# Optimization experiments

Measured on AMD Instinct MI355X. Metric: run time of the kernel, lower is better.

The kernel has to match this reference:

```python
import jax, jax.numpy as jnp
import numpy as np

# batch, net nodes/graph, vnr nodes/graph, hidden, static feats, vnr feats, vnf types, value out
B, NN, NV, H, FS, FV, T, O = 64, 1000, 10, 128, 8, 6, 8, 64
EN, EV = B * NN * 8, B * NV * 4  # total edges (avg degree 8 / 4)


def _gat(h, src, dst, W, al, ar, b):
    """dgl GATConv, num_heads=1, activation=None, allow_zero_in_degree=True."""
    n = h.shape[0]
    z = h @ W                                                    # [N,H]
    e = jax.nn.leaky_relu((z @ al)[src] + (z @ ar)[dst], 0.2)    # [E]
    emax = jax.ops.segment_max(e, dst, num_segments=n)
    ee = jnp.exp(e - emax[dst])
    alpha = ee / jax.ops.segment_sum(ee, dst, num_segments=n)[dst]
    return jax.ops.segment_sum(z[src] * alpha[:, None], dst, num_segments=n) + b


def _gru_cell(x, h, W_ih, W_hh, b_ih, b_hh):
    gi = x @ W_ih.T + b_ih
    gh = h @ W_hh.T + b_hh
    ir, iz, in_ = jnp.split(gi, 3, axis=-1)
    hr, hz, hn = jnp.split(gh, 3, axis=-1)
    r = jax.nn.sigmoid(ir + hr)
    z = jax.nn.sigmoid(iz + hz)
    n = jnp.tanh(in_ + r * hn)
    return (1.0 - z) * n + z * h


def _forward(static_feat, vnr_feat, nmask,
             Ws1, als1, ars1, bs1, Ws2, als2, ars2, bs2, Ws3, als3, ars3, bs3,
             Wv1, alv1, arv1, bv1, Wv2, alv2, arv2, bv2, Wv3, alv3, arv3, bv3,
             W_attn, v_attn, W_ih, W_hh, b_ih, b_hh, h0, W_out, b_out,
             src_s, dst_s, src_v, dst_v, vnr_VNF, net_VNF):
    # ---- graph encoders: 3 stacked GAT layers each ----
    hs = _gat(static_feat, src_s, dst_s, Ws1, als1, ars1, bs1)
    hs = _gat(hs, src_s, dst_s, Ws2, als2, ars2, bs2)
    hs = _gat(hs, src_s, dst_s, Ws3, als3, ars3, bs3)            # [B*NN,H]
    hv = _gat(vnr_feat, src_v, dst_v, Wv1, alv1, arv1, bv1)
    hv = _gat(hv, src_v, dst_v, Wv2, alv2, arv2, bv2)
    hv = _gat(hv, src_v, dst_v, Wv3, alv3, arv3, bv3)            # [B*NV,H]
    static_hidden = hs.reshape(B, NN, H).transpose(0, 2, 1)      # [B,H,NN]
    vnr_hidden = hv.reshape(B, NV, H).transpose(0, 2, 1)         # [B,H,NV]

    # ---- pointer decoder ----
    netV = net_VNF.reshape(B, NN, T)
    # mask[b,i,n] = netV[b, n, vnr_VNF[b,i]]
    masks = jnp.take_along_axis(netV[:, None, :, :], vnr_VNF[:, :, None, None], axis=3)[..., 0]  # [B,NV,NN]

    def step(h, x):
        h_new = _gru_cell(x, h, W_ih, W_hh, b_ih, b_hh)          # [B,H]
        cat = jnp.concatenate(
            [static_hidden, jnp.broadcast_to(h_new[:, :, None], (B, H, NN))], axis=1)  # [B,2H,NN]
        attn = jnp.einsum('h,bhn->bn', v_attn,
                          jnp.tanh(jnp.einsum('hk,bkn->bhn', W_attn, cat)))
        return h_new, attn

    h0b = jnp.broadcast_to(h0, (B, H))
    xs = vnr_hidden.transpose(2, 0, 1)                            # [NV,B,H]
    _, attns = jax.lax.scan(step, h0b, xs)                        # [NV,B,NN]
    pi = (attns.transpose(1, 0, 2) + jnp.log(masks.astype(jnp.float32))).reshape(B, -1)

    # ---- value head ----
    nm = nmask.reshape(B, NV)
    y1 = (vnr_hidden.transpose(0, 2, 1) * nm[:, :, None]).sum(1) / nm.sum(1, keepdims=True)
    y2 = static_hidden.mean(2)
    val = jnp.concatenate([y1, y2], axis=1) @ W_out.T + b_out     # [B,O]
    return pi, val


def setup_inputs() -> dict:
    key = jax.random.key(0)
    ks = iter(jax.random.split(key, 60))

    def nrm(shape, fan):
        return jax.random.normal(next(ks), shape, jnp.float32) / np.sqrt(fan).astype(np.float32)

    inp = {
        'static_feat': jax.random.normal(next(ks), (B * NN, FS), jnp.float32),
        'vnr_feat': jax.random.normal(next(ks), (B * NV, FV), jnp.float32),
        'nmask': jnp.ones((B * NV,), jnp.float32),
    }
    for pfx, fin in (('s1', FS), ('s2', H), ('s3', H), ('v1', FV), ('v2', H), ('v3', H)):
        inp['W' + pfx] = nrm((fin, H), fin)
        inp['al' + pfx] = nrm((H,), H)
        inp['ar' + pfx] = nrm((H,), H)
        inp['b' + pfx] = jnp.zeros((H,), jnp.float32)
    inp['W_attn'] = nrm((H, 2 * H), 2 * H)
    inp['v_attn'] = nrm((H,), H)
    inp['W_ih'] = nrm((3 * H, H), H)
    inp['W_hh'] = nrm((3 * H, H), H)
    inp['b_ih'] = jnp.zeros((3 * H,), jnp.float32)
    inp['b_hh'] = jnp.zeros((3 * H,), jnp.float32)
    inp['h0'] = jnp.zeros((H,), jnp.float32)
    inp['W_out'] = nrm((O, 2 * H), 2 * H)
    inp['b_out'] = jnp.zeros((O,), jnp.float32)
    inp['src_s'] = jax.random.randint(next(ks), (EN,), 0, B * NN)
    inp['dst_s'] = jax.random.randint(next(ks), (EN,), 0, B * NN)
    inp['src_v'] = jax.random.randint(next(ks), (EV,), 0, B * NV)
    inp['dst_v'] = jax.random.randint(next(ks), (EV,), 0, B * NV)
    inp['vnr_VNF'] = jax.random.randint(next(ks), (B, NV), 0, T)
    inp['net_VNF'] = jnp.ones((B * NN, T), jnp.int32)
    return inp


def reference(static_feat, vnr_feat, nmask,
              Ws1, als1, ars1, bs1, Ws2, als2, ars2, bs2, Ws3, als3, ars3, bs3,
              Wv1, alv1, arv1, bv1, Wv2, alv2, arv2, bv2, Wv3, alv3, arv3, bv3,
              W_attn, v_attn, W_ih, W_hh, b_ih, b_hh, h0, W_out, b_out,
              src_s, dst_s, src_v, dst_v, vnr_VNF, net_VNF):
    return _forward(static_feat, vnr_feat, nmask,
                    Ws1, als1, ars1, bs1, Ws2, als2, ars2, bs2, Ws3, als3, ars3, bs3,
                    Wv1, alv1, arv1, bv1, Wv2, alv2, arv2, bv2, Wv3, alv3, arv3, bv3,
                    W_attn, v_attn, W_ih, W_hh, b_ih, b_hh, h0, W_out, b_out,
                    src_s, dst_s, src_v, dst_v, vnr_VNF, net_VNF)
```

## Files before the change

### kernel.cpp

```cpp
#include <hip/hip_runtime.h>
#include <hip/hip_bf16.h>
#include <math.h>

#define B_   64
#define NN_  1000
#define NV_  10
#define H_   128
#define FS_  8
#define FV_  6
#define T_   8
#define O_   64
#define EN_  512000
#define EV_  2560
#define NS_  (B_*NN_)
#define NVT_ (B_*NV_)

typedef __attribute__((ext_vector_type(8))) short short8v;
typedef __attribute__((ext_vector_type(4))) float floatx4;

__device__ __forceinline__ float fast_rcp(float x) { return __builtin_amdgcn_rcpf(x); }
__device__ __forceinline__ float fast_tanh(float x) {
  return 1.f - 2.f*fast_rcp(1.f + __expf(2.f*x));
}
__device__ __forceinline__ float fast_sigmoid(float x) {
  return fast_rcp(1.f + __expf(-x));
}
__device__ __forceinline__ unsigned short bf16_rne(float x) {
  unsigned u = __float_as_uint(x);
  return (unsigned short)((u + 0x7FFFu + ((u >> 16) & 1u)) >> 16);
}
__device__ __forceinline__ float bf16_tof(unsigned short b) {
  return __uint_as_float(((unsigned)b) << 16);
}
__device__ __forceinline__ float dot4(float4 a, float4 b) {
  return a.x*b.x + a.y*b.y + a.z*b.z + a.w*b.w;
}
__device__ __forceinline__ float lrelu02(float e) {
  return (e > 0.f) ? e : 0.2f*e;
}

__global__ __launch_bounds__(256) void k_count(const int* dst, int E, int* counts) {
  int i = blockIdx.x*256 + threadIdx.x;
  if (i < E) atomicAdd(&counts[dst[i]], 1);
}

__global__ __launch_bounds__(1024) void k_scan(const int* cnt, int n, int* rowptr) {
  __shared__ int sums[1024];
  int t = threadIdx.x;
  int v = (t < n) ? cnt[t] : 0;
  sums[t] = v;
  __syncthreads();
  for (int offd = 1; offd < 1024; offd <<= 1) {
    int u = (t >= offd) ? sums[t-offd] : 0;
    __syncthreads();
    sums[t] += u;
    __syncthreads();
  }
  if (t < n) rowptr[t] = sums[t] - v;
  if (t == n-1) rowptr[n] = sums[t];
}

__global__ __launch_bounds__(256) void k_scan_local(const int* cnt, int n, int* out, int* bsum) {
  __shared__ int s[256];
  int t = threadIdx.x; int i = blockIdx.x*256 + t;
  int v = (i < n) ? cnt[i] : 0;
  s[t] = v; __syncthreads();
  #pragma unroll
  for (int o = 1; o < 256; o <<= 1) {
    int u = (t >= o) ? s[t-o] : 0; __syncthreads();
    s[t] += u; __syncthreads();
  }
  if (i < n) out[i] = s[t] - v;
  if (t == 255) bsum[blockIdx.x] = s[255];
}

__global__ __launch_bounds__(256) void k_scan_bsum(int* bsum, int nb) {
  __shared__ int s[256];
  int t = threadIdx.x;
  int v = (t < nb) ? bsum[t] : 0;
  s[t] = v; __syncthreads();
  #pragma unroll
  for (int o = 1; o < 256; o <<= 1) {
    int u = (t >= o) ? s[t-o] : 0; __syncthreads();
    s[t] += u; __syncthreads();
  }
  if (t < nb) bsum[t] = s[t] - v;
}

__global__ __launch_bounds__(256) void k_scan_add(int* out, const int* bsum, int n, int E) {
  int i = blockIdx.x*256 + threadIdx.x;
  if (i < n) out[i] += bsum[blockIdx.x];
  if (i == 0) out[n] = E;
}

__global__ __launch_bounds__(256) void k_scatter(const int* src, const int* dst, int E,
                                                 const int* rowptr, int* cursor,
                                                 unsigned short* srcp) {
  int i = blockIdx.x*256 + threadIdx.x;
  if (i >= E) return;
  int d = dst[i];
  int pos = rowptr[d] + atomicAdd(&cursor[d], 1);
  srcp[pos] = (unsigned short)src[i];
}

__global__ __launch_bounds__(256) void k_aggregate_v(int nNodes, const int* __restrict__ rowptr,
    const unsigned short* __restrict__ srcp, const float* __restrict__ el,
    const float* __restrict__ er, const float* __restrict__ z,
    const float* __restrict__ bias, float* __restrict__ out) {
  int w = (blockIdx.x*256 + threadIdx.x) >> 6;
  int lane = threadIdx.x & 63;
  if (w >= nNodes) return;
  int beg = rowptr[w], end = rowptr[w+1];
  float erw = er[w];
  float a0 = 0.f, a1 = 0.f, wsum = 0.f;
  for (int i = beg; i < end; ++i) {
    int sI = srcp[i];
    float wt = __expf(lrelu02(el[sI] + erw));
    float2 zz = *(const float2*)(z + (size_t)sI*H_ + lane*2);
    a0 += wt*zz.x; a1 += wt*zz.y; wsum += wt;
  }
  float inv = (end > beg) ? fast_rcp(wsum) : 0.f;
  float2 o;
  o.x = a0*inv + bias[lane*2];
  o.y = a1*inv + bias[lane*2 + 1];
  *(float2*)(out + (size_t)w*H_ + lane*2) = o;
}

__global__ __launch_bounds__(256) void k_aggregate_split(int nNodes, const int* __restrict__ rowptr,
    const unsigned short* __restrict__ srcp, const float* __restrict__ el, const float* __restrict__ er,
    const unsigned short* __restrict__ z, const float* __restrict__ bias,
    unsigned short* __restrict__ outHi, unsigned short* __restrict__ outLo) {
  int w = (blockIdx.x*256 + threadIdx.x) >> 6;
  int lane = threadIdx.x & 63;
  if (w >= nNodes) return;
  int beg = rowptr[w], end = rowptr[w+1];
  float erw = er[w];
  float a0 = 0.f, a1 = 0.f, wsum = 0.f;
  int i = beg;
  for (; i + 8 <= end; i += 8) {
    int sI[8]; float lv[8]; ushort2 q[8];
    #pragma unroll
    for (int u = 0; u < 8; ++u) sI[u] = srcp[i+u];
    #pragma unroll
    for (int u = 0; u < 8; ++u) lv[u] = el[sI[u]];
    #pragma unroll
    for (int u = 0; u < 8; ++u) q[u] = *(const ushort2*)(z + (size_t)sI[u]*H_ + lane*2);
    #pragma unroll
    for (int u = 0; u < 8; ++u) {
      float wt = __expf(lrelu02(lv[u] + erw));
      a0 += wt*bf16_tof(q[u].x);
      a1 += wt*bf16_tof(q[u].y);
      wsum += wt;
    }
  }
  for (; i < end; ++i) {
    int sI = srcp[i];
    float wt = __expf(lrelu02(el[sI] + erw));
    ushort2 q = *(const ushort2*)(z + (size_t)sI*H_ + lane*2);
    a0 += wt*bf16_tof(q.x); a1 += wt*bf16_tof(q.y); wsum += wt;
  }
  float inv = (end > beg) ? fast_rcp(wsum) : 0.f;
  float o0 = a0*inv + bias[lane*2];
  float o1 = a1*inv + bias[lane*2 + 1];
  unsigned short h0 = bf16_rne(o0), h1 = bf16_rne(o1);
  unsigned short l0 = bf16_rne(o0 - bf16_tof(h0)), l1 = bf16_rne(o1 - bf16_tof(h1));
  ushort2 hv; hv.x = h0; hv.y = h1;
  ushort2 lv; lv.x = l0; lv.y = l1;
  *(ushort2*)(outHi + (size_t)w*H_ + lane*2) = hv;
  *(ushort2*)(outLo + (size_t)w*H_ + lane*2) = lv;
}

__global__ __launch_bounds__(256) void k_prep(const float* W_ih, const float* Ws2,
                                              const float* Ws3, const float* W_attn,
                                              float* WTih,
                                              unsigned short* WS2hi, unsigned short* WS2lo,
                                              unsigned short* WS3hi, unsigned short* WS3lo,
                                              unsigned short* WAhi, unsigned short* WAlo) {
  int idx = blockIdx.x*256 + threadIdx.x;
  int task = blockIdx.y;
  if (task == 0) {
    if (idx < 128*384) {
      int k = idx / 384, j = idx - k*384;
      WTih[idx] = W_ih[(size_t)j*128 + k];
    }
  } else {
    if (idx >= 128*128) return;
    int j = idx >> 7, k = idx & 127;
    float v; unsigned short *hi, *lo;
    if (task == 1)      { v = Ws2[(size_t)k*128 + j];    hi = WS2hi; lo = WS2lo; }
    else if (task == 2) { v = Ws3[(size_t)k*128 + j];    hi = WS3hi; lo = WS3lo; }
    else                { v = W_attn[(size_t)j*256 + k]; hi = WAhi;  lo = WAlo;  }
    unsigned short h = bf16_rne(v);
    hi[idx] = h; lo[idx] = bf16_rne(v - bf16_tof(h));
  }
}

__global__ __launch_bounds__(256) void k_mfma_gemm(
    const unsigned short* __restrict__ Ahi, const unsigned short* __restrict__ Alo,
    const unsigned short* __restrict__ WThi, const unsigned short* __restrict__ WTlo,
    float* __restrict__ C, unsigned short* __restrict__ Cb,
    const float* __restrict__ al, const float* __restrict__ ar,
    float* __restrict__ el, float* __restrict__ er) {
  __shared__ unsigned short lAhi[64*136];
  __shared__ unsigned short lAlo[64*136];
  __shared__ float redl[4][64];
  __shared__ float redr[4][64];
  int t = threadIdx.x;
  int row0 = blockIdx.x * 64;
  int wid = t >> 6, lane = t & 63;
  int g = lane >> 4, c = lane & 15;

  #pragma unroll
  for (int i = 0; i < 4; ++i) {
    int m = t + 256*i;
    int r = m >> 4;
    int kc = (m & 15) * 8;
    *(short8v*)(lAhi + r*136 + kc) = *(const short8v*)(Ahi + (size_t)(row0 + r)*H_ + kc);
    *(short8v*)(lAlo + r*136 + kc) = *(const short8v*)(Alo + (size_t)(row0 + r)*H_ + kc);
  }

  short8v bhi[2][4], blo[2][4];
  #pragma unroll
  for (int ct = 0; ct < 2; ++ct) {
    int col = wid*32 + ct*16 + c;
    #pragma unroll
    for (int kb = 0; kb < 4; ++kb) {
      size_t o = (size_t)col*H_ + kb*32 + g*8;
      bhi[ct][kb] = *(const short8v*)(WThi + o);
      blo[ct][kb] = *(const short8v*)(WTlo + o);
    }
  }

  floatx4 acc[4][2];
  #pragma unroll
  for (int rt = 0; rt < 4; ++rt)
    #pragma unroll
    for (int ct = 0; ct < 2; ++ct)
      acc[rt][ct] = (floatx4){0.f, 0.f, 0.f, 0.f};

  __syncthreads();

  #pragma unroll
  for (int kb = 0; kb < 4; ++kb) {
    short8v ahi[4], alo[4];
    #pragma unroll
    for (int rt = 0; rt < 4; ++rt) {
      int r = rt*16 + c;
      ahi[rt] = *(const short8v*)(lAhi + r*136 + kb*32 + g*8);
      alo[rt] = *(const short8v*)(lAlo + r*136 + kb*32 + g*8);
    }
    #pragma unroll
    for (int rt = 0; rt < 4; ++rt)
      #pragma unroll
      for (int ct = 0; ct < 2; ++ct) {
        acc[rt][ct] = __builtin_amdgcn_mfma_f32_16x16x32_bf16(ahi[rt], bhi[ct][kb], acc[rt][ct], 0, 0, 0);
        acc[rt][ct] = __builtin_amdgcn_mfma_f32_16x16x32_bf16(alo[rt], bhi[ct][kb], acc[rt][ct], 0, 0, 0);
        acc[rt][ct] = __builtin_amdgcn_mfma_f32_16x16x32_bf16(ahi[rt], blo[ct][kb], acc[rt][ct], 0, 0, 0);
      }
  }

  #pragma unroll
  for (int rt = 0; rt < 4; ++rt)
    #pragma unroll
    for (int i = 0; i < 4; ++i) {
      int row = row0 + rt*16 + g*4 + i;
      if (Cb) {
        unsigned short* cr = Cb + (size_t)row*H_ + wid*32;
        cr[c]      = bf16_rne(acc[rt][0][i]);
        cr[16 + c] = bf16_rne(acc[rt][1][i]);
      } else {
        float* cr = C + (size_t)row*H_ + wid*32;
        cr[c]      = acc[rt][0][i];
        cr[16 + c] = acc[rt][1][i];
      }
    }

  if (el) {
    float av0 = al[wid*32 + c], av1 = al[wid*32 + 16 + c];
    float rv0 = ar[wid*32 + c], rv1 = ar[wid*32 + 16 + c];
    #pragma unroll
    for (int rt = 0; rt < 4; ++rt)
      #pragma unroll
      for (int i = 0; i < 4; ++i) {
        float pl = acc[rt][0][i]*av0 + acc[rt][1][i]*av1;
        float pr = acc[rt][0][i]*rv0 + acc[rt][1][i]*rv1;
        pl += __shfl_xor(pl, 1, 64); pl += __shfl_xor(pl, 2, 64);
        pl += __shfl_xor(pl, 4, 64); pl += __shfl_xor(pl, 8, 64);
        pr += __shfl_xor(pr, 1, 64); pr += __shfl_xor(pr, 2, 64);
        pr += __shfl_xor(pr, 4, 64); pr += __shfl_xor(pr, 8, 64);
        if (c == 0) { redl[wid][rt*16 + g*4 + i] = pl; redr[wid][rt*16 + g*4 + i] = pr; }
      }
    __syncthreads();
    if (t < 64) {
      el[row0 + t] = redl[0][t] + redl[1][t] + redl[2][t] + redl[3][t];
      er[row0 + t] = redr[0][t] + redr[1][t] + redr[2][t] + redr[3][t];
    }
  }
}

__global__ __launch_bounds__(256) void k_gemm(const float* A, int M, int K, int N,
                                              const float* W, const float* bias,
                                              float* C, unsigned short* Cb,
                                              const float* al, const float* ar,
                                              float* el, float* er) {
  __shared__ float Ws_[64*128];
  __shared__ float As_[16*128];
  __shared__ float redl[16][17];
  __shared__ float redr[16][17];
  int t = threadIdx.x;
  int j0 = blockIdx.y * 128;
  int row0 = blockIdx.x * 16;
  for (int l = t; l < 16*K; l += 256) {
    int r = l / K, k = l - r*K;
    int row = row0 + r;
    As_[r*K + k] = (row < M) ? A[(size_t)row*K + k] : 0.f;
  }
  int jg = t & 15, r = t >> 4;
  float acc[8];
  #pragma unroll
  for (int q = 0; q < 8; ++q) acc[q] = 0.f;
  for (int kc = 0; kc < K; kc += 64) {
    int kl = min(64, K - kc);
    __syncthreads();
    for (int l = t; l < (kl << 7); l += 256) {
      int k = l >> 7, j = l & 127;
      int jj = j0 + j;
      Ws_[l] = (jj < N) ? W[(size_t)(kc + k)*N + jj] : 0.f;
    }
    __syncthreads();
    for (int k = 0; k < kl; ++k) {
      float a = As_[r*K + kc + k];
      const float* wr = &Ws_[(k << 7) + jg*8];
      #pragma unroll
      for (int q = 0; q < 8; ++q) acc[q] += a * wr[q];
    }
  }
  int row = row0 + r;
  if (row < M) {
    if (Cb) {
      unsigned short* crow = Cb + (size_t)row*N + j0 + jg*8;
      #pragma unroll
      for (int q = 0; q < 8; ++q) {
        int j = j0 + jg*8 + q;
        if (j < N) crow[q] = bf16_rne(acc[q] + (bias ? bias[j] : 0.f));
      }
    } else {
      float* crow = C + (size_t)row*N + j0 + jg*8;
      #pragma unroll
      for (int q = 0; q < 8; ++q) {
        int j = j0 + jg*8 + q;
// ... 86 lines not shown
  int b = blockIdx.y;
  int t = threadIdx.x;
  for (int i = t; i < 1280; i += 256) {
    int s = i >> 7, k = i & 127;
    a2s[s][k] = 2.f*A2[((size_t)s*B_ + b)*H_ + k];
  }
  if (t < 128) vv2s[t] = 2.f*v_attn[t];
  __syncthreads();
  int nl = t >> 2, p = t & 3;
  int n = blockIdx.x*64 + nl;
  if (n >= NN_) return;
  size_t g = (size_t)b*NN_ + n;
  const float4* arow = (const float4*)(A1 + g*H_ + p*32);
  float4 a[8], w2[8];
  #pragma unroll
  for (int kk = 0; kk < 8; ++kk) {
    float4 av = arow[kk];
    a[kk] = make_float4(2.f*av.x, 2.f*av.y, 2.f*av.z, 2.f*av.w);
    w2[kk] = *(const float4*)(&vv2s[p*32 + kk*4]);
  }
  float vsum = 0.f;
  #pragma unroll
  for (int kk = 0; kk < 8; ++kk)
    vsum += (w2[kk].x + w2[kk].y) + (w2[kk].z + w2[kk].w);
  vsum *= 0.5f;
  float acc[10];
  #pragma unroll
  for (int s = 0; s < 10; ++s) {
    const float* a2r = &a2s[s][p*32];
    float sum2 = 0.f;
    #pragma unroll
    for (int kk = 0; kk < 8; ++kk) {
      float4 c = *(const float4*)(a2r + kk*4);
      sum2 = fmaf(w2[kk].x, fast_rcp(1.f + __expf(a[kk].x + c.x)), sum2);
      sum2 = fmaf(w2[kk].y, fast_rcp(1.f + __expf(a[kk].y + c.y)), sum2);
      sum2 = fmaf(w2[kk].z, fast_rcp(1.f + __expf(a[kk].z + c.z)), sum2);
      sum2 = fmaf(w2[kk].w, fast_rcp(1.f + __expf(a[kk].w + c.w)), sum2);
    }
    acc[s] = vsum - sum2;
  }
  #pragma unroll
  for (int s = 0; s < 10; ++s) {
    acc[s] += __shfl_xor(acc[s], 1, 64);
    acc[s] += __shfl_xor(acc[s], 2, 64);
  }
  if (p == 0) {
    #pragma unroll
    for (int s = 0; s < 10; ++s) {
      int vnf = vnr_VNF[b*NV_ + s];
      int m   = net_VNF[g*T_ + vnf];
      pi[(size_t)b*(NV_*NN_) + (size_t)s*NN_ + n] = acc[s] + __logf((float)m);
    }
  }
}

__global__ __launch_bounds__(128) void k_y2s(const unsigned short* hi, const unsigned short* lo,
                                             float* y2) {
  int b = blockIdx.x, slice = blockIdx.y, h = threadIdx.x;
  int n0 = slice*125, n1 = n0 + 125;
  float s = 0.f;
  for (int n = n0; n < n1; ++n) {
    size_t idx = ((size_t)b*NN_ + n)*H_ + h;
    s += bf16_tof(hi[idx]) + bf16_tof(lo[idx]);
  }
  atomicAdd(&y2[b*H_ + h], s);
}

__global__ __launch_bounds__(128) void k_value(const float* __restrict__ Hv,
                                               const float* __restrict__ nmask,
                                               const float* __restrict__ y2,
                                               const float* __restrict__ W_out,
                                               const float* __restrict__ b_out,
                                               float* __restrict__ val) {
  __shared__ float y1s[128];
  int b = blockIdx.x, t = threadIdx.x;
  float s = 0.f, d = 0.f;
  #pragma unroll
  for (int i = 0; i < NV_; ++i) {
    float m = nmask[b*NV_ + i];
    s += Hv[(size_t)(b*NV_ + i)*H_ + t]*m;
    d += m;
  }
  y1s[t] = s/d;
  __syncthreads();
  if (t < 64) {
    const float* w = W_out + (size_t)t*256;
    float acc = b_out[t];
    for (int h = 0; h < H_; ++h)
      acc += y1s[h]*w[h] + (y2[b*H_ + h]*(1.f/1000.f))*w[128 + h];
    val[b*O_ + t] = acc;
  }
}

extern "C" void kernel_launch(void* const* d_in, const int* in_sizes, int n_in,
                              void* d_out, int out_size, void* d_ws, size_t ws_size,
                              hipStream_t stream) {
  (void)in_sizes; (void)n_in; (void)out_size; (void)ws_size;
  const float* static_feat = (const float*)d_in[0];
  const float* vnr_feat    = (const float*)d_in[1];
  const float* nmask       = (const float*)d_in[2];
  const float* Ws1 = (const float*)d_in[3];  const float* als1 = (const float*)d_in[4];
  const float* ars1 = (const float*)d_in[5]; const float* bs1 = (const float*)d_in[6];
  const float* Ws2 = (const float*)d_in[7];  const float* als2 = (const float*)d_in[8];
  const float* ars2 = (const float*)d_in[9]; const float* bs2 = (const float*)d_in[10];
  const float* Ws3 = (const float*)d_in[11]; const float* als3 = (const float*)d_in[12];
  const float* ars3 = (const float*)d_in[13]; const float* bs3 = (const float*)d_in[14];
  const float* Wv1 = (const float*)d_in[15]; const float* alv1 = (const float*)d_in[16];
  const float* arv1 = (const float*)d_in[17]; const float* bv1 = (const float*)d_in[18];
  const float* Wv2 = (const float*)d_in[19]; const float* alv2 = (const float*)d_in[20];
  const float* arv2 = (const float*)d_in[21]; const float* bv2 = (const float*)d_in[22];
  const float* Wv3 = (const float*)d_in[23]; const float* alv3 = (const float*)d_in[24];
  const float* arv3 = (const float*)d_in[25]; const float* bv3 = (const float*)d_in[26];
  const float* W_attn = (const float*)d_in[27];
  const float* v_attn = (const float*)d_in[28];
  const float* W_ih = (const float*)d_in[29];
  const float* W_hh = (const float*)d_in[30];
  const float* b_ih = (const float*)d_in[31];
  const float* b_hh = (const float*)d_in[32];
  const float* h0   = (const float*)d_in[33];
  const float* W_out = (const float*)d_in[34];
  const float* b_out = (const float*)d_in[35];
  const int* src_s = (const int*)d_in[36];
  const int* dst_s = (const int*)d_in[37];
  const int* src_v = (const int*)d_in[38];
  const int* dst_v = (const int*)d_in[39];
  const int* vnr_VNF = (const int*)d_in[40];
  const int* net_VNF = (const int*)d_in[41];

  char* ws = (char*)d_ws;
  size_t off = 0;
  auto alloc = [&](size_t bytes) -> char* {
    off = (off + 255) & ~(size_t)255;
    char* p = ws + off;
    off += bytes;
    return p;
  };
  float* Z    = (float*)alloc((size_t)NS_*H_*4);
  unsigned short* Zb   = (unsigned short*)alloc((size_t)NS_*H_*2);
  unsigned short* HsHi = (unsigned short*)alloc((size_t)NS_*H_*2);
  unsigned short* HsLo = (unsigned short*)alloc((size_t)NS_*H_*2);
  float* Zv   = (float*)alloc((size_t)NVT_*H_*4);
  float* Hv   = (float*)alloc((size_t)NVT_*H_*4);
  float* el_s = (float*)alloc((size_t)NS_*4);
  float* er_s = (float*)alloc((size_t)NS_*4);
  float* el_v = (float*)alloc((size_t)NVT_*4);
  float* er_v = (float*)alloc((size_t)NVT_*4);
  size_t zcount = (size_t)NS_ + NS_ + NVT_ + NVT_ + B_*H_;
  char* zb = alloc(zcount*4);
  int*   counts_s = (int*)zb;
  int*   cursor_s = counts_s + NS_;
  int*   counts_v = cursor_s + NS_;
  int*   cursor_v = counts_v + NVT_;
  float* y2buf    = (float*)(cursor_v + NVT_);
  int* rowptr_s = (int*)alloc((size_t)(NS_+1)*4);
  int* rowptr_v = (int*)alloc((size_t)(NVT_+1)*4);
  int* bsum     = (int*)alloc((size_t)256*4);
  unsigned short* srcp_s = (unsigned short*)alloc((size_t)EN_*2);
  unsigned short* srcp_v = (unsigned short*)alloc((size_t)EV_*2);
  unsigned short* WS2hi = (unsigned short*)alloc((size_t)H_*H_*2);
  unsigned short* WS2lo = (unsigned short*)alloc((size_t)H_*H_*2);
  unsigned short* WS3hi = (unsigned short*)alloc((size_t)H_*H_*2);
  unsigned short* WS3lo = (unsigned short*)alloc((size_t)H_*H_*2);
  unsigned short* WAhi  = (unsigned short*)alloc((size_t)H_*H_*2);
  unsigned short* WAlo  = (unsigned short*)alloc((size_t)H_*H_*2);
  float* WTih   = (float*)alloc((size_t)H_*384*4);
  float* GI     = (float*)alloc((size_t)NVT_*384*4);
  float* A2     = (float*)alloc((size_t)NV_*B_*H_*4);

  float* pi  = (float*)d_out;
  float* val = pi + (size_t)B_*NV_*NN_;

  hipMemsetAsync(zb, 0, zcount*4, stream);

  k_prep<<<dim3(192, 4), 256, 0, stream>>>(W_ih, Ws2, Ws3, W_attn, WTih,
                                           WS2hi, WS2lo, WS3hi, WS3lo, WAhi, WAlo);

  k_count<<<EN_/256, 256, 0, stream>>>(dst_s, EN_, counts_s);
  k_count<<<EV_/256, 256, 0, stream>>>(dst_v, EV_, counts_v);
  k_scan_local<<<250, 256, 0, stream>>>(counts_s, NS_, rowptr_s, bsum);
  k_scan_bsum<<<1, 256, 0, stream>>>(bsum, 250);
  k_scan_add<<<250, 256, 0, stream>>>(rowptr_s, bsum, NS_, EN_);
  k_scan<<<1, 1024, 0, stream>>>(counts_v, NVT_, rowptr_v);
  k_scatter<<<EN_/256, 256, 0, stream>>>(src_s, dst_s, EN_, rowptr_s, cursor_s, srcp_s);
  k_scatter<<<EV_/256, 256, 0, stream>>>(src_v, dst_v, EV_, rowptr_v, cursor_v, srcp_v);

  dim3 gemmV(NVT_/16, 1);
  int aggS = (NS_ + 3)/4, aggV = (NVT_ + 3)/4;

  k_gemm<<<dim3(NS_/16, 1), 256, 0, stream>>>(static_feat, NS_, FS_, H_, Ws1, nullptr,
                                              nullptr, Zb, als1, ars1, el_s, er_s);
  k_aggregate_split<<<aggS, 256, 0, stream>>>(NS_, rowptr_s, srcp_s, el_s, er_s, Zb, bs1, HsHi, HsLo);
  k_mfma_gemm<<<NS_/64, 256, 0, stream>>>(HsHi, HsLo, WS2hi, WS2lo, nullptr, Zb, als2, ars2, el_s, er_s);
  k_aggregate_split<<<aggS, 256, 0, stream>>>(NS_, rowptr_s, srcp_s, el_s, er_s, Zb, bs2, HsHi, HsLo);
  k_mfma_gemm<<<NS_/64, 256, 0, stream>>>(HsHi, HsLo, WS3hi, WS3lo, nullptr, Zb, als3, ars3, el_s, er_s);
  k_aggregate_split<<<aggS, 256, 0, stream>>>(NS_, rowptr_s, srcp_s, el_s, er_s, Zb, bs3, HsHi, HsLo);

  k_gemm<<<gemmV, 256, 0, stream>>>(vnr_feat, NVT_, FV_, H_, Wv1, nullptr, Zv, nullptr, alv1, arv1, el_v, er_v);
  k_aggregate_v<<<aggV, 256, 0, stream>>>(NVT_, rowptr_v, srcp_v, el_v, er_v, Zv, bv1, Hv);
  k_gemm<<<gemmV, 256, 0, stream>>>(Hv, NVT_, H_, H_, Wv2, nullptr, Zv, nullptr, alv2, arv2, el_v, er_v);
  k_aggregate_v<<<aggV, 256, 0, stream>>>(NVT_, rowptr_v, srcp_v, el_v, er_v, Zv, bv2, Hv);
  k_gemm<<<gemmV, 256, 0, stream>>>(Hv, NVT_, H_, H_, Wv3, nullptr, Zv, nullptr, alv3, arv3, el_v, er_v);
  k_aggregate_v<<<aggV, 256, 0, stream>>>(NVT_, rowptr_v, srcp_v, el_v, er_v, Zv, bv3, Hv);

  k_gemm<<<dim3(NVT_/16, 3), 256, 0, stream>>>(Hv, NVT_, H_, 384, WTih, b_ih, GI, nullptr,
                                               nullptr, nullptr, nullptr, nullptr);
  k_mfma_gemm<<<NS_/64, 256, 0, stream>>>(HsHi, HsLo, WAhi, WAlo, Z, nullptr,
                                          nullptr, nullptr, nullptr, nullptr);
  k_decoder<<<B_, 512, 0, stream>>>(GI, W_hh, b_hh, W_attn, h0, A2);
  k_attn3<<<dim3(16, B_), 256, 0, stream>>>(Z, A2, v_attn, vnr_VNF, net_VNF, pi);

  k_y2s<<<dim3(B_, 8), 128, 0, stream>>>(HsHi, HsLo, y2buf);
  k_value<<<B_, 128, 0, stream>>>(Hv, nmask, y2buf, W_out, b_out, val);
}
```

Before: 448.8 us.

## Fuse GAT aggregation with next-layer MFMA GEMM and merge graph setup kernels

Each static-graph GAT aggregation now writes its hi/lo bf16 split output into LDS and immediately runs the next layer's split-bf16 MFMA GEMM, with the el/er projections, in the same block. This removes the HsHi/HsLo round trip through global memory. The last aggregation is fused with the attention-projection GEMM and also accumulates the per-graph node sums via atomics, which replaces the separate k_y2s pass. The VNR encoder moves to the same fused MFMA path, and the edge count, scan and scatter kernels for both graphs are merged to cut launches. In exchange each wave processes 16 nodes serially before the GEMM, which lowers parallelism in the gather phase and may lengthen the critical path.

```diff
diff --git a/kernel.cpp b/kernel.cpp
--- a/kernel.cpp
+++ b/kernel.cpp
@@ -39,25 +39,11 @@
   return (e > 0.f) ? e : 0.2f*e;
 }
 
-__global__ __launch_bounds__(256) void k_count(const int* dst, int E, int* counts) {
+__global__ __launch_bounds__(256) void k_count2(const int* dst_s, const int* dst_v,
+                                                int* counts_s, int* counts_v) {
   int i = blockIdx.x*256 + threadIdx.x;
-  if (i < E) atomicAdd(&counts[dst[i]], 1);
-}
-
-__global__ __launch_bounds__(1024) void k_scan(const int* cnt, int n, int* rowptr) {
-  __shared__ int sums[1024];
-  int t = threadIdx.x;
-  int v = (t < n) ? cnt[t] : 0;
-  sums[t] = v;
-  __syncthreads();
-  for (int offd = 1; offd < 1024; offd <<= 1) {
-    int u = (t >= offd) ? sums[t-offd] : 0;
-    __syncthreads();
-    sums[t] += u;
-    __syncthreads();
-  }
-  if (t < n) rowptr[t] = sums[t] - v;
-  if (t == n-1) rowptr[n] = sums[t];
+  if (i < EN_) atomicAdd(&counts_s[dst_s[i]], 1);
+  else if (i < EN_ + EV_) atomicAdd(&counts_v[dst_v[i - EN_]], 1);
 }
 
 __global__ __launch_bounds__(256) void k_scan_local(const int* cnt, int n, int* out, int* bsum) {
@@ -74,17 +60,28 @@
   if (t == 255) bsum[blockIdx.x] = s[255];
 }
 
-__global__ __launch_bounds__(256) void k_scan_bsum(int* bsum, int nb) {
-  __shared__ int s[256];
+__global__ __launch_bounds__(1024) void k_scan_small(int* bsum, int nb,
+                                                     const int* cntv, int* rowptr_v, int nv, int Ev) {
+  __shared__ int sums[1024];
   int t = threadIdx.x;
-  int v = (t < nb) ? bsum[t] : 0;
-  s[t] = v; __syncthreads();
-  #pragma unroll
-  for (int o = 1; o < 256; o <<= 1) {
-    int u = (t >= o) ? s[t-o] : 0; __syncthreads();
-    s[t] += u; __syncthreads();
-  }
-  if (t < nb) bsum[t] = s[t] - v;
+  if (blockIdx.x == 0) {
+    int v = (t < nb) ? bsum[t] : 0;
+    sums[t] = v; __syncthreads();
+    for (int o = 1; o < 1024; o <<= 1) {
+      int u = (t >= o) ? sums[t-o] : 0; __syncthreads();
+      sums[t] += u; __syncthreads();
+    }
+    if (t < nb) bsum[t] = sums[t] - v;
+  } else {
+    int v = (t < nv) ? cntv[t] : 0;
+    sums[t] = v; __syncthreads();
+    for (int o = 1; o < 1024; o <<= 1) {
+      int u = (t >= o) ? sums[t-o] : 0; __syncthreads();
+      sums[t] += u; __syncthreads();
+    }
+    if (t < nv) rowptr_v[t] = sums[t] - v;
+    if (t == nv-1) rowptr_v[nv] = sums[t];
+  }
 }
 
 __global__ __launch_bounds__(256) void k_scan_add(int* out, const int* bsum, int n, int E) {
@@ -93,19 +90,230 @@
   if (i == 0) out[n] = E;
 }
 
-__global__ __launch_bounds__(256) void k_scatter(const int* src, const int* dst, int E,
-                                                 const int* rowptr, int* cursor,
-                                                 unsigned short* srcp) {
+__global__ __launch_bounds__(256) void k_scatter2(const int* src_s, const int* dst_s,
+                                                  const int* src_v, const int* dst_v,
+                                                  const int* rowptr_s, const int* rowptr_v,
+                                                  int* cursor_s, int* cursor_v,
+                                                  unsigned short* srcp_s, unsigned short* srcp_v) {
   int i = blockIdx.x*256 + threadIdx.x;
-  if (i >= E) return;
-  int d = dst[i];
-  int pos = rowptr[d] + atomicAdd(&cursor[d], 1);
-  srcp[pos] = (unsigned short)src[i];
-}
-
-__global__ __launch_bounds__(256) void k_aggregate_v(int nNodes, const int* __restrict__ rowptr,
+  if (i < EN_) {
+    int d = dst_s[i];
+    int pos = rowptr_s[d] + atomicAdd(&cursor_s[d], 1);
+    srcp_s[pos] = (unsigned short)src_s[i];
+  } else if (i < EN_ + EV_) {
+    int j = i - EN_;
+    int d = dst_v[j];
+    int pos = rowptr_v[d] + atomicAdd(&cursor_v[d], 1);
+    srcp_v[pos] = (unsigned short)src_v[j];
+  }
+}
+
+__global__ __launch_bounds__(256) void k_prep(const float* W_ih, const float* Ws2,
+                                              const float* Ws3, const float* W_attn,
+                                              const float* Wv2, const float* Wv3,
+                                              float* WTih,
+                                              unsigned short* WS2hi, unsigned short* WS2lo,
+                                              unsigned short* WS3hi, unsigned short* WS3lo,
+                                              unsigned short* WAhi, unsigned short* WAlo,
+                                              unsigned short* WV2hi, unsigned short* WV2lo,
+                                              unsigned short* WV3hi, unsigned short* WV3lo) {
+  int idx = blockIdx.x*256 + threadIdx.x;
+  int task = blockIdx.y;
+  if (task == 0) {
+    if (idx < 128*384) {
+      int k = idx / 384, j = idx - k*384;
+      WTih[idx] = W_ih[(size_t)j*128 + k];
+    }
+  } else {
+    if (idx >= 128*128) return;
+    int j = idx >> 7, k = idx & 127;
+    float v; unsigned short *hi, *lo;
+    if (task == 1)      { v = Ws2[(size_t)k*128 + j];    hi = WS2hi; lo = WS2lo; }
+    else if (task == 2) { v = Ws3[(size_t)k*128 + j];    hi = WS3hi; lo = WS3lo; }
+    else if (task == 3) { v = W_attn[(size_t)j*256 + k]; hi = WAhi;  lo = WAlo;  }
+    else if (task == 4) { v = Wv2[(size_t)k*128 + j];    hi = WV2hi; lo = WV2lo; }
+    else                { v = Wv3[(size_t)k*128 + j];    hi = WV3hi; lo = WV3lo; }
+    unsigned short h = bf16_rne(v);
+    hi[idx] = h; lo[idx] = bf16_rne(v - bf16_tof(h));
+  }
+}
+
+__global__ __launch_bounds__(256) void k_agg_mfma(
+    const int* __restrict__ rowptr, const unsigned short* __restrict__ srcp,
+    const float* __restrict__ el_in, const float* __restrict__ er_in,
+    const unsigned short* __restrict__ z_in, const float* __restrict__ bias,
+    const unsigned short* __restrict__ WThi, const unsigned short* __restrict__ WTlo,
+    unsigned short* __restrict__ zb_out, float* __restrict__ Cf,
+    const float* __restrict__ al, const float* __restrict__ ar,
+    float* __restrict__ el_out, float* __restrict__ er_out,
+    float* __restrict__ y2) {
+  __shared__ unsigned short lAhi[64*136];
+  __shared__ unsigned short lAlo[64*136];
+  __shared__ float redl[4][64];
+  __shared__ float redr[4][64];
+  int t = threadIdx.x;
+  int row0 = blockIdx.x * 64;
+  int wid = t >> 6, lane = t & 63;
+  int g = lane >> 4, c = lane & 15;
+
+  float b0 = bias[lane*2], b1 = bias[lane*2 + 1];
+  float y2s0 = 0.f, y2s1 = 0.f; int y2b = -1;
+
+  for (int j = 0; j < 8; ++j) {
+    int wA = row0 + wid*16 + 2*j;
+    int wB = wA + 1;
+    int begA = rowptr[wA], endA = rowptr[wA+1];
+    int begB = rowptr[wB], endB = rowptr[wB+1];
+    float erA = er_in[wA], erB = er_in[wB];
+    float a0A = 0.f, a1A = 0.f, wsA = 0.f;
+    float a0B = 0.f, a1B = 0.f, wsB = 0.f;
+    int iA = begA, iB = begB;
+    while (iA < endA || iB < endB) {
+      int sA[8], sB[8];
+      #pragma unroll
+      for (int u = 0; u < 8; ++u) {
+        sA[u] = (iA + u < endA) ? (int)srcp[iA + u] : 0;
+        sB[u] = (iB + u < endB) ? (int)srcp[iB + u] : 0;
+      }
+      float lA[8], lB[8];
+      #pragma unroll
+      for (int u = 0; u < 8; ++u) { lA[u] = el_in[sA[u]]; lB[u] = el_in[sB[u]]; }
+      ushort2 qA[8], qB[8];
+      #pragma unroll
+      for (int u = 0; u < 8; ++u) {
+        qA[u] = *(const ushort2*)(z_in + (size_t)sA[u]*H_ + lane*2);
+        qB[u] = *(const ushort2*)(z_in + (size_t)sB[u]*H_ + lane*2);
+      }
+      #pragma unroll
+      for (int u = 0; u < 8; ++u) {
+        float wtA = (iA + u < endA) ? __expf(lrelu02(lA[u] + erA)) : 0.f;
+        float wtB = (iB + u < endB) ? __expf(lrelu02(lB[u] + erB)) : 0.f;
+        a0A += wtA*bf16_tof(qA[u].x); a1A += wtA*bf16_tof(qA[u].y); wsA += wtA;
+        a0B += wtB*bf16_tof(qB[u].x); a1B += wtB*bf16_tof(qB[u].y); wsB += wtB;
+      }
+      iA += 8; iB += 8;
+    }
+    float invA = (endA > begA) ? fast_rcp(wsA) : 0.f;
+    float invB = (endB > begB) ? fast_rcp(wsB) : 0.f;
+    float o0A = a0A*invA + b0, o1A = a1A*invA + b1;
+    float o0B = a0B*invB + b0, o1B = a1B*invB + b1;
+    int rA = wid*16 + 2*j;
+    unsigned short hA0 = bf16_rne(o0A), hA1 = bf16_rne(o1A);
+    unsigned short hB0 = bf16_rne(o0B), hB1 = bf16_rne(o1B);
+    ushort2 hvA; hvA.x = hA0; hvA.y = hA1;
+    ushort2 lvA; lvA.x = bf16_rne(o0A - bf16_tof(hA0)); lvA.y = bf16_rne(o1A - bf16_tof(hA1));
+    ushort2 hvB; hvB.x = hB0; hvB.y = hB1;
+    ushort2 lvB; lvB.x = bf16_rne(o0B - bf16_tof(hB0)); lvB.y = bf16_rne(o1B - bf16_tof(hB1));
+    *(ushort2*)(lAhi + rA*136 + lane*2) = hvA;
+    *(ushort2*)(lAlo + rA*136 + lane*2) = lvA;
+    *(ushort2*)(lAhi + (rA+1)*136 + lane*2) = hvB;
+    *(ushort2*)(lAlo + (rA+1)*136 + lane*2) = lvB;
+    if (y2) {
+      int bA = wA / NN_;
+      if (bA != y2b) {
+        if (y2b >= 0) {
+          atomicAdd(&y2[y2b*H_ + lane*2], y2s0);
+          atomicAdd(&y2[y2b*H_ + lane*2 + 1], y2s1);
+        }
+        y2b = bA; y2s0 = 0.f; y2s1 = 0.f;
+      }
+      y2s0 += o0A; y2s1 += o1A;
+      int bB = wB / NN_;
+      if (bB != y2b) {
+        atomicAdd(&y2[y2b*H_ + lane*2], y2s0);
+        atomicAdd(&y2[y2b*H_ + lane*2 + 1], y2s1);
+        y2b = bB; y2s0 = 0.f; y2s1 = 0.f;
+      }
+      y2s0 += o0B; y2s1 += o1B;
+    }
+  }
+  if (y2 && y2b >= 0) {
+    atomicAdd(&y2[y2b*H_ + lane*2], y2s0);
+    atomicAdd(&y2[y2b*H_ + lane*2 + 1], y2s1);
+  }
+
+  short8v bhi[2][4], blo[2][4];
+  #pragma unroll
+  for (int ct = 0; ct < 2; ++ct) {
+    int col = wid*32 + ct*16 + c;
+    #pragma unroll
+    for (int kb = 0; kb < 4; ++kb) {
+      size_t o = (size_t)col*H_ + kb*32 + g*8;
+      bhi[ct][kb] = *(const short8v*)(WThi + o);
+      blo[ct][kb] = *(const short8v*)(WTlo + o);
+    }
+  }
+
+  floatx4 acc[4][2];
+  #pragma unroll
+  for (int rt = 0; rt < 4; ++rt)
+    #pragma unroll
+    for (int ct = 0; ct < 2; ++ct)
+      acc[rt][ct] = (floatx4){0.f, 0.f, 0.f, 0.f};
+
+  __syncthreads();
+
+  #pragma unroll
+  for (int kb = 0; kb < 4; ++kb) {
+    short8v ahi[4], alo[4];
+    #pragma unroll
+    for (int rt = 0; rt < 4; ++rt) {
+      int r = rt*16 + c;
+      ahi[rt] = *(const short8v*)(lAhi + r*136 + kb*32 + g*8);
+      alo[rt] = *(const short8v*)(lAlo + r*136 + kb*32 + g*8);
+    }
+    #pragma unroll
+    for (int rt = 0; rt < 4; ++rt)
+      #pragma unroll
+      for (int ct = 0; ct < 2; ++ct) {
+        acc[rt][ct] = __builtin_amdgcn_mfma_f32_16x16x32_bf16(ahi[rt], bhi[ct][kb], acc[rt][ct], 0, 0, 0);
+        acc[rt][ct] = __builtin_amdgcn_mfma_f32_16x16x32_bf16(alo[rt], bhi[ct][kb], acc[rt][ct], 0, 0, 0);
+        acc[rt][ct] = __builtin_amdgcn_mfma_f32_16x16x32_bf16(ahi[rt], blo[ct][kb], acc[rt][ct], 0, 0, 0);
+      }
+  }
+
+  #pragma unroll
+  for (int rt = 0; rt < 4; ++rt)
+    #pragma unroll
+    for (int i = 0; i < 4; ++i) {
+      int row = row0 + rt*16 + g*4 + i;
+      if (zb_out) {
+        unsigned short* cr = zb_out + (size_t)row*H_ + wid*32;
+        cr[c]      = bf16_rne(acc[rt][0][i]);
+        cr[16 + c] = bf16_rne(acc[rt][1][i]);
+      } else {
+        float* cr = Cf + (size_t)row*H_ + wid*32;
+        cr[c]      = acc[rt][0][i];
+        cr[16 + c] = acc[rt][1][i];
+      }
+    }
+
+  if (el_out) {
+    float av0 = al[wid*32 + c], av1 = al[wid*32 + 16 + c];
+    float rv0 = ar[wid*32 + c], rv1 = ar[wid*32 + 16 + c];
+    #pragma unroll
+    for (int rt = 0; rt < 4; ++rt)
+      #pragma unroll
+      for (int i = 0; i < 4; ++i) {
+        float pl = acc[rt][0][i]*av0 + acc[rt][1][i]*av1;
+        float pr = acc[rt][0][i]*rv0 + acc[rt][1][i]*rv1;
+        pl += __shfl_xor(pl, 1, 64); pl += __shfl_xor(pl, 2, 64);
+        pl += __shfl_xor(pl, 4, 64); pl += __shfl_xor(pl, 8, 64);
+        pr += __shfl_xor(pr, 1, 64); pr += __shfl_xor(pr, 2, 64);
+        pr += __shfl_xor(pr, 4, 64); pr += __shfl_xor(pr, 8, 64);
+        if (c == 0) { redl[wid][rt*16 + g*4 + i] = pl; redr[wid][rt*16 + g*4 + i] = pr; }
+      }
+    __syncthreads();
+    if (t < 64) {
+      el_out[row0 + t] = redl[0][t] + redl[1][t] + redl[2][t] + redl[3][t];
+      er_out[row0 + t] = redr[0][t] + redr[1][t] + redr[2][t] + redr[3][t];
+    }
+  }
+}
+
+__global__ __launch_bounds__(256) void k_aggregate_f(int nNodes, const int* __restrict__ rowptr,
     const unsigned short* __restrict__ srcp, const float* __restrict__ el,
-    const float* __restrict__ er, const float* __restrict__ z,
+    const float* __restrict__ er, const unsigned short* __restrict__ z,
     const float* __restrict__ bias, float* __restrict__ out) {
   int w = (blockIdx.x*256 + threadIdx.x) >> 6;
   int lane = threadIdx.x & 63;
@@ -116,186 +324,14 @@
   for (int i = beg; i < end; ++i) {
     int sI = srcp[i];
     float wt = __expf(lrelu02(el[sI] + erw));
-    float2 zz = *(const float2*)(z + (size_t)sI*H_ + lane*2);
-    a0 += wt*zz.x; a1 += wt*zz.y; wsum += wt;
+    ushort2 q = *(const ushort2*)(z + (size_t)sI*H_ + lane*2);
+    a0 += wt*bf16_tof(q.x); a1 += wt*bf16_tof(q.y); wsum += wt;
   }
   float inv = (end > beg) ? fast_rcp(wsum) : 0.f;
   float2 o;
   o.x = a0*inv + bias[lane*2];
   o.y = a1*inv + bias[lane*2 + 1];
   *(float2*)(out + (size_t)w*H_ + lane*2) = o;
-}
-
-__global__ __launch_bounds__(256) void k_aggregate_split(int nNodes, const int* __restrict__ rowptr,
-    const unsigned short* __restrict__ srcp, const float* __restrict__ el, const float* __restrict__ er,
-    const unsigned short* __restrict__ z, const float* __restrict__ bias,
-    unsigned short* __restrict__ outHi, unsigned short* __restrict__ outLo) {
-  int w = (blockIdx.x*256 + threadIdx.x) >> 6;
-  int lane = threadIdx.x & 63;
-  if (w >= nNodes) return;
-  int beg = rowptr[w], end = rowptr[w+1];
-  float erw = er[w];
-  float a0 = 0.f, a1 = 0.f, wsum = 0.f;
-  int i = beg;
-  for (; i + 8 <= end; i += 8) {
-    int sI[8]; float lv[8]; ushort2 q[8];
-    #pragma unroll
-    for (int u = 0; u < 8; ++u) sI[u] = srcp[i+u];
-    #pragma unroll
-    for (int u = 0; u < 8; ++u) lv[u] = el[sI[u]];
-    #pragma unroll
-    for (int u = 0; u < 8; ++u) q[u] = *(const ushort2*)(z + (size_t)sI[u]*H_ + lane*2);
-    #pragma unroll
-    for (int u = 0; u < 8; ++u) {
-      float wt = __expf(lrelu02(lv[u] + erw));
-      a0 += wt*bf16_tof(q[u].x);
-      a1 += wt*bf16_tof(q[u].y);
-      wsum += wt;
-    }
-  }
-  for (; i < end; ++i) {
-    int sI = srcp[i];
-    float wt = __expf(lrelu02(el[sI] + erw));
-    ushort2 q = *(const ushort2*)(z + (size_t)sI*H_ + lane*2);
-    a0 += wt*bf16_tof(q.x); a1 += wt*bf16_tof(q.y); wsum += wt;
-  }
-  float inv = (end > beg) ? fast_rcp(wsum) : 0.f;
-  float o0 = a0*inv + bias[lane*2];
-  float o1 = a1*inv + bias[lane*2 + 1];
-  unsigned short h0 = bf16_rne(o0), h1 = bf16_rne(o1);
-  unsigned short l0 = bf16_rne(o0 - bf16_tof(h0)), l1 = bf16_rne(o1 - bf16_tof(h1));
-  ushort2 hv; hv.x = h0; hv.y = h1;
-  ushort2 lv; lv.x = l0; lv.y = l1;
-  *(ushort2*)(outHi + (size_t)w*H_ + lane*2) = hv;
-  *(ushort2*)(outLo + (size_t)w*H_ + lane*2) = lv;
-}
-
-__global__ __launch_bounds__(256) void k_prep(const float* W_ih, const float* Ws2,
-                                              const float* Ws3, const float* W_attn,
-                                              float* WTih,
-                                              unsigned short* WS2hi, unsigned short* WS2lo,
-                                              unsigned short* WS3hi, unsigned short* WS3lo,
-                                              unsigned short* WAhi, unsigned short* WAlo) {
-  int idx = blockIdx.x*256 + threadIdx.x;
-  int task = blockIdx.y;
-  if (task == 0) {
-    if (idx < 128*384) {
-      int k = idx / 384, j = idx - k*384;
-      WTih[idx] = W_ih[(size_t)j*128 + k];
-    }
-  } else {
-    if (idx >= 128*128) return;
-    int j = idx >> 7, k = idx & 127;
-    float v; unsigned short *hi, *lo;
-    if (task == 1)      { v = Ws2[(size_t)k*128 + j];    hi = WS2hi; lo = WS2lo; }
-    else if (task == 2) { v = Ws3[(size_t)k*128 + j];    hi = WS3hi; lo = WS3lo; }
-    else                { v = W_attn[(size_t)j*256 + k]; hi = WAhi;  lo = WAlo;  }
-    unsigned short h = bf16_rne(v);
-    hi[idx] = h; lo[idx] = bf16_rne(v - bf16_tof(h));
-  }
-}
-
-__global__ __launch_bounds__(256) void k_mfma_gemm(
-    const unsigned short* __restrict__ Ahi, const unsigned short* __restrict__ Alo,
-    const unsigned short* __restrict__ WThi, const unsigned short* __restrict__ WTlo,
-    float* __restrict__ C, unsigned short* __restrict__ Cb,
-    const float* __restrict__ al, const float* __restrict__ ar,
-    float* __restrict__ el, float* __restrict__ er) {
-  __shared__ unsigned short lAhi[64*136];
-  __shared__ unsigned short lAlo[64*136];
-  __shared__ float redl[4][64];
-  __shared__ float redr[4][64];
-  int t = threadIdx.x;
-  int row0 = blockIdx.x * 64;
-  int wid = t >> 6, lane = t & 63;
-  int g = lane >> 4, c = lane & 15;
-
-  #pragma unroll
-  for (int i = 0; i < 4; ++i) {
-    int m = t + 256*i;
-    int r = m >> 4;
-    int kc = (m & 15) * 8;
-    *(short8v*)(lAhi + r*136 + kc) = *(const short8v*)(Ahi + (size_t)(row0 + r)*H_ + kc);
-    *(short8v*)(lAlo + r*136 + kc) = *(const short8v*)(Alo + (size_t)(row0 + r)*H_ + kc);
-  }
-
-  short8v bhi[2][4], blo[2][4];
-  #pragma unroll
-  for (int ct = 0; ct < 2; ++ct) {
-    int col = wid*32 + ct*16 + c;
-    #pragma unroll
-    for (int kb = 0; kb < 4; ++kb) {
-      size_t o = (size_t)col*H_ + kb*32 + g*8;
-      bhi[ct][kb] = *(const short8v*)(WThi + o);
-      blo[ct][kb] = *(const short8v*)(WTlo + o);
-    }
-  }
-
-  floatx4 acc[4][2];
-  #pragma unroll
-  for (int rt = 0; rt < 4; ++rt)
-    #pragma unroll
-    for (int ct = 0; ct < 2; ++ct)
-      acc[rt][ct] = (floatx4){0.f, 0.f, 0.f, 0.f};
-
-  __syncthreads();
-
-  #pragma unroll
-  for (int kb = 0; kb < 4; ++kb) {
-    short8v ahi[4], alo[4];
-    #pragma unroll
-    for (int rt = 0; rt < 4; ++rt) {
-      int r = rt*16 + c;
-      ahi[rt] = *(const short8v*)(lAhi + r*136 + kb*32 + g*8);
-      alo[rt] = *(const short8v*)(lAlo + r*136 + kb*32 + g*8);
-    }
-    #pragma unroll
-    for (int rt = 0; rt < 4; ++rt)
-      #pragma unroll
-      for (int ct = 0; ct < 2; ++ct) {
-        acc[rt][ct] = __builtin_amdgcn_mfma_f32_16x16x32_bf16(ahi[rt], bhi[ct][kb], acc[rt][ct], 0, 0, 0);
-        acc[rt][ct] = __builtin_amdgcn_mfma_f32_16x16x32_bf16(alo[rt], bhi[ct][kb], acc[rt][ct], 0, 0, 0);
-        acc[rt][ct] = __builtin_amdgcn_mfma_f32_16x16x32_bf16(ahi[rt], blo[ct][kb], acc[rt][ct], 0, 0, 0);
-      }
-  }
-
-  #pragma unroll
-  for (int rt = 0; rt < 4; ++rt)
-    #pragma unroll
-    for (int i = 0; i < 4; ++i) {
-      int row = row0 + rt*16 + g*4 + i;
-      if (Cb) {
-        unsigned short* cr = Cb + (size_t)row*H_ + wid*32;
-        cr[c]      = bf16_rne(acc[rt][0][i]);
-        cr[16 + c] = bf16_rne(acc[rt][1][i]);
-      } else {
-        float* cr = C + (size_t)row*H_ + wid*32;
-        cr[c]      = acc[rt][0][i];
-        cr[16 + c] = acc[rt][1][i];
-      }
-    }
-
-  if (el) {
-    float av0 = al[wid*32 + c], av1 = al[wid*32 + 16 + c];
-    float rv0 = ar[wid*32 + c], rv1 = ar[wid*32 + 16 + c];
-    #pragma unroll
-    for (int rt = 0; rt < 4; ++rt)
-      #pragma unroll
-      for (int i = 0; i < 4; ++i) {
-        float pl = acc[rt][0][i]*av0 + acc[rt][1][i]*av1;
-        float pr = acc[rt][0][i]*rv0 + acc[rt][1][i]*rv1;
-        pl += __shfl_xor(pl, 1, 64); pl += __shfl_xor(pl, 2, 64);
-        pl += __shfl_xor(pl, 4, 64); pl += __shfl_xor(pl, 8, 64);
-        pr += __shfl_xor(pr, 1, 64); pr += __shfl_xor(pr, 2, 64);
-        pr += __shfl_xor(pr, 4, 64); pr += __shfl_xor(pr, 8, 64);
-        if (c == 0) { redl[wid][rt*16 + g*4 + i] = pl; redr[wid][rt*16 + g*4 + i] = pr; }
-      }
-    __syncthreads();
-    if (t < 64) {
-      el[row0 + t] = redl[0][t] + redl[1][t] + redl[2][t] + redl[3][t];
-      er[row0 + t] = redr[0][t] + redr[1][t] + redr[2][t] + redr[3][t];
-    }
-  }
 }
 
 __global__ __launch_bounds__(256) void k_gemm(const float* A, int M, int K, int N,
@@ -488,18 +524,6 @@
       pi[(size_t)b*(NV_*NN_) + (size_t)s*NN_ + n] = acc[s] + __logf((float)m);
     }
   }
-}
-
-__global__ __launch_bounds__(128) void k_y2s(const unsigned short* hi, const unsigned short* lo,
-                                             float* y2) {
-  int b = blockIdx.x, slice = blockIdx.y, h = threadIdx.x;
-  int n0 = slice*125, n1 = n0 + 125;
-  float s = 0.f;
-  for (int n = n0; n < n1; ++n) {
-    size_t idx = ((size_t)b*NN_ + n)*H_ + h;
-    s += bf16_tof(hi[idx]) + bf16_tof(lo[idx]);
-  }
-  atomicAdd(&y2[b*H_ + h], s);
 }
 
 __global__ __launch_bounds__(128) void k_value(const float* __restrict__ Hv,
@@ -572,15 +596,19 @@
     return p;
   };
   float* Z    = (float*)alloc((size_t)NS_*H_*4);
-  unsigned short* Zb   = (unsigned short*)alloc((size_t)NS_*H_*2);
-  unsigned short* HsHi = (unsigned short*)alloc((size_t)NS_*H_*2);
-  unsigned short* HsLo = (unsigned short*)alloc((size_t)NS_*H_*2);
-  float* Zv   = (float*)alloc((size_t)NVT_*H_*4);
+  unsigned short* Zb0 = (unsigned short*)alloc((size_t)NS_*H_*2);
+  unsigned short* Zb1 = (unsigned short*)alloc((size_t)NS_*H_*2);
+  unsigned short* Zbv0 = (unsigned short*)alloc((size_t)NVT_*H_*2);
+  unsigned short* Zbv1 = (unsigned short*)alloc((size_t)NVT_*H_*2);
   float* Hv   = (float*)alloc((size_t)NVT_*H_*4);
-  float* el_s = (float*)alloc((size_t)NS_*4);
-  float* er_s = (float*)alloc((size_t)NS_*4);
-  float* el_v = (float*)alloc((size_t)NVT_*4);
-  float* er_v = (float*)alloc((size_t)NVT_*4);
+  float* el_a = (float*)alloc((size_t)NS_*4);
+  float* er_a = (float*)alloc((size_t)NS_*4);
+  float* el_b = (float*)alloc((size_t)NS_*4);
+  float* er_b = (float*)alloc((size_t)NS_*4);
+  float* elv_a = (float*)alloc((size_t)NVT_*4);
+  float* erv_a = (float*)alloc((size_t)NVT_*4);
+  float* elv_b = (float*)alloc((size_t)NVT_*4);
+  float* erv_b = (float*)alloc((size_t)NVT_*4);
   size_t zcount = (size_t)NS_ + NS_ + NVT_ + NVT_ + B_*H_;
   char* zb = alloc(zcount*4);
   int*   counts_s = (int*)zb;
@@ -591,14 +619,18 @@
   int* rowptr_s = (int*)alloc((size_t)(NS_+1)*4);
   int* rowptr_v = (int*)alloc((size_t)(NVT_+1)*4);
   int* bsum     = (int*)alloc((size_t)256*4);
-  unsigned short* srcp_s = (unsigned short*)alloc((size_t)EN_*2);
-  unsigned short* srcp_v = (unsigned short*)alloc((size_t)EV_*2);
+  unsigned short* srcp_s = (unsigned short*)alloc((size_t)(EN_+8)*2);
+  unsigned short* srcp_v = (unsigned short*)alloc((size_t)(EV_+8)*2);
   unsigned short* WS2hi = (unsigned short*)alloc((size_t)H_*H_*2);
   unsigned short* WS2lo = (unsigned short*)alloc((size_t)H_*H_*2);
   unsigned short* WS3hi = (unsigned short*)alloc((size_t)H_*H_*2);
   unsigned short* WS3lo = (unsigned short*)alloc((size_t)H_*H_*2);
   unsigned short* WAhi  = (unsigned short*)alloc((size_t)H_*H_*2);
   unsigned short* WAlo  = (unsigned short*)alloc((size_t)H_*H_*2);
+  unsigned short* WV2hi = (unsigned short*)alloc((size_t)H_*H_*2);
+  unsigned short* WV2lo = (unsigned short*)alloc((size_t)H_*H_*2);
+  unsigned short* WV3hi = (unsigned short*)alloc((size_t)H_*H_*2);
+  unsigned short* WV3lo = (unsigned short*)alloc((size_t)H_*H_*2);
   float* WTih   = (float*)alloc((size_t)H_*384*4);
   float* GI     = (float*)alloc((size_t)NVT_*384*4);
   float* A2     = (float*)alloc((size_t)NV_*B_*H_*4);
@@ -608,43 +640,46 @@
 
   hipMemsetAsync(zb, 0, zcount*4, stream);
 
-  k_prep<<<dim3(192, 4), 256, 0, stream>>>(W_ih, Ws2, Ws3, W_attn, WTih,
-                                           WS2hi, WS2lo, WS3hi, WS3lo, WAhi, WAlo);
-
-  k_count<<<EN_/256, 256, 0, stream>>>(dst_s, EN_, counts_s);
-  k_count<<<EV_/256, 256, 0, stream>>>(dst_v, EV_, counts_v);
+  k_prep<<<dim3(192, 6), 256, 0, stream>>>(W_ih, Ws2, Ws3, W_attn, Wv2, Wv3, WTih,
+                                           WS2hi, WS2lo, WS3hi, WS3lo, WAhi, WAlo,
+                                           WV2hi, WV2lo, WV3hi, WV3lo);
+
+  int edgeBlocks = (EN_ + EV_ + 255)/256;
+  k_count2<<<edgeBlocks, 256, 0, stream>>>(dst_s, dst_v, counts_s, counts_v);
   k_scan_local<<<250, 256, 0, stream>>>(counts_s, NS_, rowptr_s, bsum);
-  k_scan_bsum<<<1, 256, 0, stream>>>(bsum, 250);
+  k_scan_small<<<2, 1024, 0, stream>>>(bsum, 250, counts_v, rowptr_v, NVT_, EV_);
   k_scan_add<<<250, 256, 0, stream>>>(rowptr_s, bsum, NS_, EN_);
-  k_scan<<<1, 1024, 0, stream>>>(counts_v, NVT_, rowptr_v);
-  k_scatter<<<EN_/256, 256, 0, stream>>>(src_s, dst_s, EN_, rowptr_s, cursor_s, srcp_s);
-  k_scatter<<<EV_/256, 256, 0, stream>>>(src_v, dst_v, EV_, rowptr_v, cursor_v, srcp_v);
-
-  dim3 gemmV(NVT_/16, 1);
-  int aggS = (NS_ + 3)/4, aggV = (NVT_ + 3)/4;
+  k_scatter2<<<edgeBlocks, 256, 0, stream>>>(src_s, dst_s, src_v, dst_v,
+                                             rowptr_s, rowptr_v, cursor_s, cursor_v,
+                                             srcp_s, srcp_v);
 
   k_gemm<<<dim3(NS_/16, 1), 256, 0, stream>>>(static_feat, NS_, FS_, H_, Ws1, nullptr,
-                                              nullptr, Zb, als1, ars1, el_s, er_s);
-  k_aggregate_split<<<aggS, 256, 0, stream>>>(NS_, rowptr_s, srcp_s, el_s, er_s, Zb, bs1, HsHi, HsLo);
-  k_mfma_gemm<<<NS_/64, 256, 0, stream>>>(HsHi, HsLo, WS2hi, WS2lo, nullptr, Zb, als2, ars2, el_s, er_s);
-  k_aggregate_split<<<aggS, 256, 0, stream>>>(NS_, rowptr_s, srcp_s, el_s, er_s, Zb, bs2, HsHi, HsLo);
-  k_mfma_gemm<<<NS_/64, 256, 0, stream>>>(HsHi, HsLo, WS3hi, WS3lo, nullptr, Zb, als3, ars3, el_s, er_s);
-  k_aggregate_split<<<aggS, 256, 0, stream>>>(NS_, rowptr_s, srcp_s, el_s, er_s, Zb, bs3, HsHi, HsLo);
-
-  k_gemm<<<gemmV, 256, 0, stream>>>(vnr_feat, NVT_, FV_, H_, Wv1, nullptr, Zv, nullptr, alv1, arv1, el_v, er_v);
-  k_aggregate_v<<<aggV, 256, 0, stream>>>(NVT_, rowptr_v, srcp_v, el_v, er_v, Zv, bv1, Hv);
-  k_gemm<<<gemmV, 256, 0, stream>>>(Hv, NVT_, H_, H_, Wv2, nullptr, Zv, nullptr, alv2, arv2, el_v, er_v);
-  k_aggregate_v<<<aggV, 256, 0, stream>>>(NVT_, rowptr_v, srcp_v, el_v, er_v, Zv, bv2, Hv);
-  k_gemm<<<gemmV, 256, 0, stream>>>(Hv, NVT_, H_, H_, Wv3, nullptr, Zv, nullptr, alv3, arv3, el_v, er_v);
-  k_aggregate_v<<<aggV, 256, 0, stream>>>(NVT_, rowptr_v, srcp_v, el_v, er_v, Zv, bv3, Hv);
+                                              nullptr, Zb0, als1, ars1, el_a, er_a);
+  k_agg_mfma<<<NS_/64, 256, 0, stream>>>(rowptr_s, srcp_s, el_a, er_a, Zb0, bs1,
+                                         WS2hi, WS2lo, Zb1, nullptr,
+                                         als2, ars2, el_b, er_b, nullptr);
+  k_agg_mfma<<<NS_/64, 256, 0, stream>>>(rowptr_s, srcp_s, el_b, er_b, Zb1, bs2,
+                                         WS3hi, WS3lo, Zb0, nullptr,
+                                         als3, ars3, el_a, er_a, nullptr);
+  k_agg_mfma<<<NS_/64, 256, 0, stream>>>(rowptr_s, srcp_s, el_a, er_a, Zb0, bs3,
+                                         WAhi, WAlo, nullptr, Z,
+                                         nullptr, nullptr, nullptr, nullptr, y2buf);
+
+  k_gemm<<<dim3(NVT_/16, 1), 256, 0, stream>>>(vnr_feat, NVT_, FV_, H_, Wv1, nullptr,
+                                               nullptr, Zbv0, alv1, arv1, elv_a, erv_a);
+  k_agg_mfma<<<NVT_/64, 256, 0, stream>>>(rowptr_v, srcp_v, elv_a, erv_a, Zbv0, bv1,
+                                          WV2hi, WV2lo, Zbv1, nullptr,
+                                          alv2, arv2, elv_b, erv_b, nullptr);
+  k_agg_mfma<<<NVT_/64, 256, 0, stream>>>(rowptr_v, srcp_v, elv_b, erv_b, Zbv1, bv2,
+                                          WV3hi, WV3lo, Zbv0, nullptr,
+                                          alv3, arv3, elv_a, erv_a, nullptr);
+  k_aggregate_f<<<(NVT_ + 3)/4, 256, 0, stream>>>(NVT_, rowptr_v, srcp_v, elv_a, erv_a,
+                                                  Zbv0, bv3, Hv);
 
   k_gemm<<<dim3(NVT_/16, 3), 256, 0, stream>>>(Hv, NVT_, H_, 384, WTih, b_ih, GI, nullptr,
                                                nullptr, nullptr, nullptr, nullptr);
-  k_mfma_gemm<<<NS_/64, 256, 0, stream>>>(HsHi, HsLo, WAhi, WAlo, Z, nullptr,
-                                          nullptr, nullptr, nullptr, nullptr);
   k_decoder<<<B_, 512, 0, stream>>>(GI, W_hh, b_hh, W_attn, h0, A2);
   k_attn3<<<dim3(16, B_), 256, 0, stream>>>(Z, A2, v_attn, vnr_VNF, net_VNF, pi);
 
-  k_y2s<<<dim3(B_, 8), 128, 0, stream>>>(HsHi, HsLo, y2buf);
   k_value<<<B_, 128, 0, stream>>>(Hv, nmask, y2buf, W_out, b_out, val);
 }
```

Measured after the change: 548.4 us. 22.2% more time.
